# Optimization experiments

Hardware: AMD Instinct MI355X
Metric: run time of the kernel (lower is better)

Reference implementation:

```python
import jax, jax.numpy as jnp
import numpy as np
import math

DIM = 1024
ATTN_DIM = 1024
B, S = 2, 4096

def setup_inputs() -> dict:
    key = jax.random.key(0)
    k1, k2, k3 = jax.random.split(key, 3)
    x = jax.random.normal(k1, (B, S, DIM), dtype=jnp.float32)
    # qkv Linear(dim, 3*attn_dim, bias=True): weight [3*attn_dim, dim], bias [3*attn_dim]
    W_qkv = jax.random.normal(k2, (3 * ATTN_DIM, DIM), dtype=jnp.float32) * (1.0 / math.sqrt(DIM))
    b_qkv = jax.random.normal(k3, (3 * ATTN_DIM,), dtype=jnp.float32) * 0.01
    return {"x": x, "W_qkv": W_qkv, "b_qkv": b_qkv}

def reference(x, W_qkv, b_qkv):
    b, s, d = x.shape
    qkv = jnp.einsum('bsd,ed->bse', x, W_qkv) + b_qkv  # [B,S,3*attn_dim]
    q, k, v = jnp.split(qkv, 3, axis=-1)
    score = jnp.einsum('bqd,bkd->bqk', q, k)  # [B,S,S]
    # causal mask applied BEFORE scaling (matches original: -inf survives the divide)
    causal = jnp.tril(jnp.ones((s, s), dtype=bool))
    score = jnp.where(causal, score, -jnp.inf)
    attn = jax.nn.softmax(score / math.sqrt(ATTN_DIM), axis=-1)
    y = jnp.einsum('bqk,bkd->bqd', attn, v)  # [B,S,attn_dim]
    return y
```

## Files before the change

### kernel.cpp

```cpp
#include <hip/hip_runtime.h>
#include <cstdint>
#include <cstddef>

typedef __bf16 bf16;
typedef bf16 bf16x4 __attribute__((ext_vector_type(4)));
typedef bf16 bf16x8 __attribute__((ext_vector_type(8)));
typedef float f32x4 __attribute__((ext_vector_type(4)));

#define SEQ 4096
#define DIMD 1024
#define TILE_K1024 131072L
#define TILE_K4096 524288L
#define PC_BATCH   8650752L

__device__ __forceinline__ int swz(int r, int c) {
    return r * 32 + (((((c >> 3) ^ (r >> 1)) & 3)) << 3) + (c & 7);
}

__device__ __forceinline__ void async16(void* lds, const void* g) {
    __builtin_amdgcn_global_load_lds(
        (__attribute__((address_space(1))) void*)g,
        (__attribute__((address_space(3))) void*)lds,
        16, 0, 0);
}

__device__ __forceinline__ void gemm_core(
    const bf16* __restrict__ At, const bf16* __restrict__ Bt,
    int k0, int k1, f32x4 acc[4][4])
{
    __shared__ bf16 lt[2][2][4096];
    const int tid  = threadIdx.x;
    const int lane = tid & 63;
    const int wid  = tid >> 6;
    const int wm   = (wid >> 1) * 64;
    const int wn   = (wid & 1) * 64;
    const int lr   = lane & 15;
    const int q    = lane >> 4;

    int offA[4], offB[4];
#pragma unroll
    for (int mi = 0; mi < 4; ++mi) {
        const int rA = wm + mi * 16 + lr;
        offA[mi] = rA * 32 + ((((rA >> 1) ^ q) & 3) << 3);
    }
#pragma unroll
    for (int ni = 0; ni < 4; ++ni) {
        const int rB = wn + ni * 16 + lr;
        offB[ni] = rB * 32 + ((((rB >> 1) ^ q) & 3) << 3);
    }

    const int t8 = tid * 8;

#define STAGE(kk, c) do { \
        const bf16* _sa = At + (long)(kk) * 4096; \
        const bf16* _sb = Bt + (long)(kk) * 4096; \
        async16(&lt[c][0][t8],        _sa + t8); \
        async16(&lt[c][0][2048 + t8], _sa + 2048 + t8); \
        async16(&lt[c][1][t8],        _sb + t8); \
        async16(&lt[c][1][2048 + t8], _sb + 2048 + t8); \
    } while (0)

    STAGE(k0, 0);
    if (k0 + 1 < k1) STAGE(k0 + 1, 1);

    for (int kk = k0; kk < k1; ++kk) {
        const int cur = (kk - k0) & 1;
        if (kk + 1 < k1) { asm volatile("s_waitcnt vmcnt(4)" ::: "memory"); }
        else             { asm volatile("s_waitcnt vmcnt(0)" ::: "memory"); }
        __builtin_amdgcn_s_barrier();
        __builtin_amdgcn_sched_barrier(0);

        bf16x8 af[4], bfr[4];
#pragma unroll
        for (int mi = 0; mi < 4; ++mi)
            af[mi] = *(const bf16x8*)&lt[cur][0][offA[mi]];
#pragma unroll
        for (int ni = 0; ni < 4; ++ni)
            bfr[ni] = *(const bf16x8*)&lt[cur][1][offB[ni]];

        __builtin_amdgcn_s_setprio(1);
#pragma unroll
        for (int mi = 0; mi < 4; ++mi)
#pragma unroll
            for (int ni = 0; ni < 4; ++ni)
                acc[mi][ni] = __builtin_amdgcn_mfma_f32_16x16x32_bf16(
                    af[mi], bfr[ni], acc[mi][ni], 0, 0, 0);
        __builtin_amdgcn_s_setprio(0);
        __builtin_amdgcn_sched_barrier(0);
        __builtin_amdgcn_s_barrier();
        if (kk + 2 < k1) STAGE(kk + 2, cur);
    }
#undef STAGE
}

__global__ __launch_bounds__(256) void cvt_all_kernel(
    const float* __restrict__ x, const float* __restrict__ W,
    bf16* __restrict__ xt, bf16* __restrict__ wt, float* __restrict__ sums)
{
    const int g = blockIdx.x, tid = threadIdx.x;
    if (g >= 11264) { sums[(g - 11264) * 256 + tid] = 0.0f; return; }
    const float* in; bf16* out; int i;
    if (g < 8192) { in = x; out = xt; i = g * 256 + tid; }
    else          { in = W; out = wt; i = (g - 8192) * 256 + tid; }
    const float4 v = ((const float4*)in)[i];
    const int j = i * 4, row = j >> 10, col = j & 1023;
    const long o = (long)(row >> 7) * TILE_K1024 + (col >> 5) * 4096
                 + swz(row & 127, col & 31);
    bf16x4 ov = { (bf16)v.x, (bf16)v.y, (bf16)v.z, (bf16)v.w };
    *(bf16x4*)&out[o] = ov;
}

__global__ __launch_bounds__(512, 2) void qkv_gemm(
    const bf16* __restrict__ xt, const bf16* __restrict__ wt,
    const float* __restrict__ bias,
    bf16* __restrict__ Qt, bf16* __restrict__ Kt, bf16* __restrict__ Vtt)
{
    __shared__ bf16 lt[3][4][4096];

    const int b = blockIdx.x, x = b & 7, r = b >> 3;
    const int mt2 = x * 4 + r / 12, nt2 = r % 12;

    const bf16* A0 = xt + (long)(2 * mt2) * TILE_K1024;
    const bf16* A1 = A0 + TILE_K1024;
    const bf16* B0 = wt + (long)(2 * nt2) * TILE_K1024;
    const bf16* B1 = B0 + TILE_K1024;

    const int tid  = threadIdx.x;
    const int lane = tid & 63;
    const int wid  = tid >> 6;
    const int wr   = wid >> 2;
    const int wc   = wid & 3;
    const int lr   = lane & 15;
    const int q    = lane >> 4;
    const int t8   = tid * 8;

    int offA[8], offB[4];
#pragma unroll
    for (int mi = 0; mi < 8; ++mi) {
        const int rA = mi * 16 + lr;
        offA[mi] = rA * 32 + ((((rA >> 1) ^ q) & 3) << 3);
    }
#pragma unroll
    for (int ni = 0; ni < 4; ++ni) {
        const int rB = (wc & 1) * 64 + ni * 16 + lr;
        offB[ni] = rB * 32 + ((((rB >> 1) ^ q) & 3) << 3);
    }
    const int bslot = 2 + (wc >> 1);

    f32x4 acc[8][4] = {};

#define STG(kk, c) do { \
        const long ko = (long)(kk) * 4096 + t8; \
        async16(&lt[c][0][t8], A0 + ko); \
        async16(&lt[c][1][t8], A1 + ko); \
        async16(&lt[c][2][t8], B0 + ko); \
        async16(&lt[c][3][t8], B1 + ko); \
    } while (0)

    STG(0, 0); STG(1, 1); STG(2, 2);

    int cur = 0;
    for (int kk = 0; kk < 32; ++kk) {
        if      (kk + 2 < 32) { asm volatile("s_waitcnt vmcnt(8)" ::: "memory"); }
        else if (kk + 1 < 32) { asm volatile("s_waitcnt vmcnt(4)" ::: "memory"); }
        else                  { asm volatile("s_waitcnt vmcnt(0)" ::: "memory"); }
        __builtin_amdgcn_s_barrier();
        __builtin_amdgcn_sched_barrier(0);

        bf16x8 af[8], bfr[4];
#pragma unroll
        for (int mi = 0; mi < 8; ++mi)
            af[mi] = *(const bf16x8*)&lt[cur][wr][offA[mi]];
#pragma unroll
        for (int ni = 0; ni < 4; ++ni)
            bfr[ni] = *(const bf16x8*)&lt[cur][bslot][offB[ni]];

        __builtin_amdgcn_s_setprio(1);
#pragma unroll
        for (int mi = 0; mi < 8; ++mi)
#pragma unroll
            for (int ni = 0; ni < 4; ++ni)
                acc[mi][ni] = __builtin_amdgcn_mfma_f32_16x16x32_bf16(
                    af[mi], bfr[ni], acc[mi][ni], 0, 0, 0);
        __builtin_amdgcn_s_setprio(0);
        __builtin_amdgcn_sched_barrier(0);
        __builtin_amdgcn_s_barrier();
        if (kk + 3 < 32) STG(kk + 3, cur);
        cur = (cur == 2) ? 0 : cur + 1;
    }
#undef STG

    const int q4 = q * 4;
    const int bm = mt2 * 256, bn = nt2 * 256;
#pragma unroll
    for (int ni = 0; ni < 4; ++ni) {
        const int n = bn + wc * 64 + ni * 16 + lr;
        const float bv = bias[n];
#pragma unroll
        for (int mi = 0; mi < 8; ++mi) {
            const int m0 = bm + wr * 128 + mi * 16 + q4;
            if (n < 2048) {
                bf16* dst = (n < 1024) ? Qt : Kt;
                const int c = n & 1023;
#pragma unroll
                for (int rr = 0; rr < 4; ++rr) {
                    const int m = m0 + rr;
                    dst[(long)(m >> 7) * TILE_K1024 + (c >> 5) * 4096
                        + swz(m & 127, c & 31)] = (bf16)(acc[mi][ni][rr] + bv);
                }
            } else {
                const int bb = m0 >> 12, s = m0 & 4095, d = n - 2048;
                bf16x4 o = { (bf16)(acc[mi][ni][0] + bv), (bf16)(acc[mi][ni][1] + bv),
                             (bf16)(acc[mi][ni][2] + bv), (bf16)(acc[mi][ni][3] + bv) };
                *(bf16x4*)&Vtt[(long)bb * 4194304 + (long)(d >> 7) * TILE_K4096
                               + (s >> 5) * 4096 + swz(d & 127, s & 31)] = o;
            }
        }
    }
}

__global__ __launch_bounds__(256) void score_kernel(
    const bf16* __restrict__ Qt, const bf16* __restrict__ Kt,
    bf16* __restrict__ Pc, float* __restrict__ sums)
{
    const int b = blockIdx.x, x = b & 7;
    int r = b >> 3;
    const int bz = r / 66, batch = bz;
    r %= 66;
    int qt, kt;
    const int s0 = x + 1;
    if (r < s0)           { qt = x;      kt = r; }
    else if (r < 33)      { qt = 31 - x; kt = r - s0; }
    else if (r < 42 + x)  { qt = x + 8;  kt = r - 33; }
    else                  { qt = 23 - x; kt = r - 42 - x; }

    bf16* Pb = Pc + (long)bz * PC_BATCH + (long)(qt * (qt + 1) / 2 + kt) * 16384;
    float* sb = sums + (long)batch * SEQ;

    f32x4 acc[4][4] = {};
    gemm_core(Qt + (long)(batch * 32 + qt) * TILE_K1024,
              Kt + (long)(batch * 32 + kt) * TILE_K1024, 0, 32, acc);

    const int tid = threadIdx.x, lane = tid & 63, wid = tid >> 6;
    const int wm = (wid >> 1) * 64, wn = (wid & 1) * 64;
    const int lr = lane & 15, q4 = (lane >> 4) * 4;
#pragma unroll
    for (int mi = 0; mi < 4; ++mi) {
#pragma unroll
        for (int rr = 0; rr < 4; ++rr) {
            const int ql = wm + mi * 16 + q4 + rr;
            const int q  = qt * 128 + ql;
            float rsum = 0.0f;
#pragma unroll
            for (int ni = 0; ni < 4; ++ni) {
                const int kl  = wn + ni * 16 + lr;
                const int key = kt * 128 + kl;
                const float s = acc[mi][ni][rr] * 0.03125f;
                const float p = (key <= q) ? __expf(s) : 0.0f;
                const bf16 pb = (bf16)p;
                Pb[(kl >> 5) * 4096 + swz(ql, kl & 31)] = pb;
                rsum += (float)pb;
            }
            rsum += __shfl_xor(rsum, 1);
            rsum += __shfl_xor(rsum, 2);
            rsum += __shfl_xor(rsum, 4);
            rsum += __shfl_xor(rsum, 8);
            if (lr == 0) atomicAdd(&sb[q], rsum);
        }
    }
}

__device__ const unsigned char pv_sched[96] = {
     15, 125,  28,  44,  25,  54,  86,  51,  83, 112,   4,   3,
     47,  93,  60,  12,  57,  22, 118,  19, 115,  80,  36,  35,
     31,  61,  92, 122,  89, 119,  10,  41,  18,  48,   5,   2,
     63,  29, 124,  90, 121,  87,  42,   9,  50,  16,  37,  34,
     95,  46,  13,  58,  24,  55,  21, 116,  82, 113,   7,   0,
    127,  14,  45,  26,  56,  23,  53,  84, 114,  81,  39,  32,
     30, 126,  27, 123,  88,  43,  85,  52,   8,  49,   6,   1,
     62,  94,  59,  91, 120,  11, 117,  20,  40,  17,  38,  33,
};

__global__ __launch_bounds__(256) void pv_kernel(
    const bf16* __restrict__ Pc, const bf16* __restrict__ Vtt,
    const float* __restrict__ sums, float* __restrict__ Y,
    float* __restrict__ part)
{
    const int b = blockIdx.x, x = b & 7, t = b >> 3;
    const int j = t >> 3, dt = t & 7;
    const int e = pv_sched[x * 12 + j];
    const int qt = e & 31, bz = (e >> 5) & 1, c = e >> 6;
    const int full = (qt + 1) * 4, half = (qt + 1) * 2;
    int k0, k1;
    if (qt < 16) { k0 = 0; k1 = full; }
    else { k0 = c ? half : 0; k1 = c ? full : half; }
    const int batch = bz;

    f32x4 acc[4][4] = {};
    gemm_core(Pc + (long)bz * PC_BATCH + (long)(qt * (qt + 1) / 2) * 16384,
              Vtt + (long)batch * 4194304 + (long)dt * TILE_K4096, k0, k1, acc);

    const int tid = threadIdx.x, lane = tid & 63, wid = tid >> 6;
    const int wm = (wid >> 1) * 64, wn = (wid & 1) * 64;
    const int lr = lane & 15, q4 = (lane >> 4) * 4;
#pragma unroll
    for (int mi = 0; mi < 4; ++mi) {
#pragma unroll
        for (int rr = 0; rr < 4; ++rr) {
            const int q = qt * 128 + wm + mi * 16 + q4 + rr;
            const float iv = 1.0f / sums[(long)batch * SEQ + q];
#pragma unroll
            for (int ni = 0; ni < 4; ++ni) {
                const int d = dt * 128 + wn + ni * 16 + lr;
                const float v = acc[mi][ni][rr] * iv;
                if (c == 0)
                    Y[(long)batch * 4194304 + (long)q * DIMD + d] = v;
                else
                    part[(long)bz * 2097152 + (long)(q - 2048) * DIMD + d] = v;
            }
        }
    }
}

__global__ __launch_bounds__(256) void combine_kernel(
    float* __restrict__ Y, const float* __restrict__ part)
{
    const long g = (long)blockIdx.x * 256 + threadIdx.x;
    const long e4 = g * 4;
    const int bz = (int)(e4 >> 21);
    const long rem = e4 & 2097151;
    float4 a = *(const float4*)&Y[(long)bz * 4194304 + 2097152 + rem];
    const float4 p = *(const float4*)&part[e4];
    a.x += p.x; a.y += p.y; a.z += p.z; a.w += p.w;
    *(float4*)&Y[(long)bz * 4194304 + 2097152 + rem] = a;
}

extern "C" void kernel_launch(void* const* d_in, const int* in_sizes, int n_in,
                              void* d_out, int out_size, void* d_ws, size_t ws_size,
                              hipStream_t stream)
{
    const float* x    = (const float*)d_in[0];
    const float* W    = (const float*)d_in[1];
    const float* bqkv = (const float*)d_in[2];
    float* out = (float*)d_out;
    char* ws = (char*)d_ws;

    bf16* Pc   = (bf16*)ws;
    bf16* xt   = (bf16*)ws;
    bf16* wt   = (bf16*)(ws + 16 * 1024 * 1024);
    bf16* Kt   = (bf16*)(ws + 34603008);
    bf16* Vtt  = (bf16*)(ws + 51380224);
    float* sums = (float*)(ws + 68157440);
    bf16* Qt   = (bf16*)d_out;
    float* part = (float*)Kt;

    cvt_all_kernel<<<11296, 256, 0, stream>>>(x, W, xt, wt, sums);
    qkv_gemm<<<384, 512, 0, stream>>>(xt, wt, bqkv, Qt, Kt, Vtt);
    score_kernel<<<1056, 256, 0, stream>>>(Qt, Kt, Pc, sums);
    pv_kernel<<<768, 256, 0, stream>>>(Pc, Vtt, sums, out, part);
    combine_kernel<<<4096, 256, 0, stream>>>(out, part);
}
```

Measured before the change: 276.6 us.

## Restructure QKV GEMM main loop into 4-slot, half-tile interleaved pipeline

Replaces the 3-stage LDS ring in the QKV projection GEMM with a 4-slot ring. Each K-step is split into two phases that each compute half the M fragments, and the A and B global-to-LDS loads are issued separately, spread across the phases. The goal is to overlap LDS reads, async global loads and MFMA issue more finely, in the style of a ping-pong schedule, and to cut register pressure from fragment buffers. It costs more LDS (128KB per block, which may reduce occupancy under launch_bounds(512,2)) and adds more barriers per K-step.

```diff
diff --git a/kernel.cpp b/kernel.cpp
--- a/kernel.cpp
+++ b/kernel.cpp
@@ -115,7 +115,7 @@
     const float* __restrict__ bias,
     bf16* __restrict__ Qt, bf16* __restrict__ Kt, bf16* __restrict__ Vtt)
 {
-    __shared__ bf16 lt[3][4][4096];
+    __shared__ bf16 lt[4][4][4096];
 
     const int b = blockIdx.x, x = b & 7, r = b >> 3;
     const int mt2 = x * 4 + r / 12, nt2 = r % 12;
@@ -149,46 +149,59 @@
 
     f32x4 acc[8][4] = {};
 
-#define STG(kk, c) do { \
-        const long ko = (long)(kk) * 4096 + t8; \
-        async16(&lt[c][0][t8], A0 + ko); \
-        async16(&lt[c][1][t8], A1 + ko); \
-        async16(&lt[c][2][t8], B0 + ko); \
-        async16(&lt[c][3][t8], B1 + ko); \
-    } while (0)
-
-    STG(0, 0); STG(1, 1); STG(2, 2);
-
-    int cur = 0;
-    for (int kk = 0; kk < 32; ++kk) {
-        if      (kk + 2 < 32) { asm volatile("s_waitcnt vmcnt(8)" ::: "memory"); }
-        else if (kk + 1 < 32) { asm volatile("s_waitcnt vmcnt(4)" ::: "memory"); }
-        else                  { asm volatile("s_waitcnt vmcnt(0)" ::: "memory"); }
-        __builtin_amdgcn_s_barrier();
-        __builtin_amdgcn_sched_barrier(0);
-
-        bf16x8 af[8], bfr[4];
-#pragma unroll
-        for (int mi = 0; mi < 8; ++mi)
-            af[mi] = *(const bf16x8*)&lt[cur][wr][offA[mi]];
-#pragma unroll
-        for (int ni = 0; ni < 4; ++ni)
-            bfr[ni] = *(const bf16x8*)&lt[cur][bslot][offB[ni]];
-
-        __builtin_amdgcn_s_setprio(1);
-#pragma unroll
-        for (int mi = 0; mi < 8; ++mi)
-#pragma unroll
-            for (int ni = 0; ni < 4; ++ni)
-                acc[mi][ni] = __builtin_amdgcn_mfma_f32_16x16x32_bf16(
-                    af[mi], bfr[ni], acc[mi][ni], 0, 0, 0);
-        __builtin_amdgcn_s_setprio(0);
-        __builtin_amdgcn_sched_barrier(0);
-        __builtin_amdgcn_s_barrier();
-        if (kk + 3 < 32) STG(kk + 3, cur);
-        cur = (cur == 2) ? 0 : cur + 1;
-    }
-#undef STG
+#define STGA(t) do { const int _c = (t) & 3; const long _ko = (long)(t) * 4096 + t8; \
+        async16(&lt[_c][0][t8], A0 + _ko); async16(&lt[_c][1][t8], A1 + _ko); } while (0)
+#define STGB(t) do { const int _c = (t) & 3; const long _ko = (long)(t) * 4096 + t8; \
+        async16(&lt[_c][2][t8], B0 + _ko); async16(&lt[_c][3][t8], B1 + _ko); } while (0)
+
+#define PHASE(SLOT, HALF, READB, STAGECODE, ENDWAIT) do { \
+    { const bf16* _pa = &lt[SLOT][wr][0]; \
+      _Pragma("unroll") \
+      for (int _mi = 0; _mi < 4; ++_mi) \
+          af[_mi] = *(const bf16x8*)(_pa + offA[(HALF) * 4 + _mi]); } \
+    if (READB) { const bf16* _pb = &lt[SLOT][bslot][0]; \
+      _Pragma("unroll") \
+      for (int _ni = 0; _ni < 4; ++_ni) \
+          bfr[_ni] = *(const bf16x8*)(_pb + offB[_ni]); } \
+    STAGECODE; \
+    __builtin_amdgcn_sched_barrier(0); \
+    __builtin_amdgcn_s_barrier(); \
+    asm volatile("s_waitcnt lgkmcnt(0)" ::: "memory"); \
+    __builtin_amdgcn_sched_barrier(0); \
+    __builtin_amdgcn_s_setprio(1); \
+    _Pragma("unroll") \
+    for (int _mi = 0; _mi < 4; ++_mi) { \
+      _Pragma("unroll") \
+      for (int _ni = 0; _ni < 4; ++_ni) \
+        acc[(HALF) * 4 + _mi][_ni] = __builtin_amdgcn_mfma_f32_16x16x32_bf16( \
+            af[_mi], bfr[_ni], acc[(HALF) * 4 + _mi][_ni], 0, 0, 0); } \
+    __builtin_amdgcn_s_setprio(0); \
+    __builtin_amdgcn_sched_barrier(0); \
+    ENDWAIT; \
+    __builtin_amdgcn_s_barrier(); \
+} while (0)
+
+    STGA(0); STGB(0); STGA(1); STGB(1);
+    asm volatile("s_waitcnt vmcnt(4)" ::: "memory");
+    __builtin_amdgcn_s_barrier();
+
+    for (int i = 0; i < 16; ++i) {
+        const int t0 = 2 * i, t1 = t0 + 1;
+        const int s0 = t0 & 3, s1 = t1 & 3;
+        const bool more = (i < 15);
+        bf16x8 af[4], bfr[4];
+
+        PHASE(s0, 0, 1, { if (more) STGA(t0 + 2); }, {});
+        PHASE(s0, 1, 0, { if (more) STGB(t0 + 2); },
+              { if (more) { asm volatile("s_waitcnt vmcnt(4)" ::: "memory"); } \
+                else      { asm volatile("s_waitcnt vmcnt(0)" ::: "memory"); } });
+        PHASE(s1, 0, 1, { if (more) STGA(t1 + 2); }, {});
+        PHASE(s1, 1, 0, { if (more) STGB(t1 + 2); },
+              { if (more) { asm volatile("s_waitcnt vmcnt(4)" ::: "memory"); } });
+    }
+#undef PHASE
+#undef STGA
+#undef STGB
 
     const int q4 = q * 4;
     const int bm = mt2 * 256, bn = nt2 * 256;
```

Result: faster. 246.3 us (-11.0%).
